# Kernel tuning notes

Hardware: AMD Instinct MI355X
Metric: run time of the kernel (lower is better)

Reference implementation:

```python
import jax, jax.numpy as jnp
import numpy as np
from jax import lax

VOCAB, EMB, HID, NCLS, BATCH, SEQ = 32000, 512, 512, 8, 64, 512


def setup_inputs() -> dict:
    key = jax.random.key(0)
    ks = jax.random.split(key, 12)
    s = 0.05
    return {
        "x": jax.random.randint(ks[0], (BATCH, SEQ), 0, VOCAB),
        "emb": jax.random.normal(ks[1], (VOCAB, EMB), jnp.float32) * s,
        "W_ih0": jax.random.normal(ks[2], (HID, EMB), jnp.float32) * s,
        "W_hh0": jax.random.normal(ks[3], (HID, HID), jnp.float32) * s,
        "b_ih0": jax.random.normal(ks[4], (HID,), jnp.float32) * s,
        "b_hh0": jax.random.normal(ks[5], (HID,), jnp.float32) * s,
        "W_ih1": jax.random.normal(ks[6], (HID, HID), jnp.float32) * s,
        "W_hh1": jax.random.normal(ks[7], (HID, HID), jnp.float32) * s,
        "b_ih1": jax.random.normal(ks[8], (HID,), jnp.float32) * s,
        "b_hh1": jax.random.normal(ks[9], (HID,), jnp.float32) * s,
        "fc_W": jax.random.normal(ks[10], (NCLS, HID), jnp.float32) * s,
        "fc_b": jax.random.normal(ks[11], (NCLS,), jnp.float32) * s,
    }


def _rnn_layer(inp, W_ih, W_hh, b_ih, b_hh):
    # inp: [B, S, F]; tanh RNN, batch_first. Precompute input projection once.
    pre = jnp.einsum('bsf,hf->bsh', inp, W_ih) + b_ih + b_hh  # [B,S,H]
    B = inp.shape[0]
    H = W_hh.shape[0]
    h0 = jnp.zeros((B, H), inp.dtype)

    def step(h, p_t):  # p_t: [B,H]
        h = jnp.tanh(p_t + h @ W_hh.T)
        return h, h

    hT, ys = lax.scan(step, h0, pre.transpose(1, 0, 2))  # scan over time
    return ys.transpose(1, 0, 2), hT  # outputs [B,S,H], last hidden [B,H]


def reference(x, emb, W_ih0, W_hh0, b_ih0, b_hh0, W_ih1, W_hh1, b_ih1, b_hh1, fc_W, fc_b):
    xe = emb[x]  # [B,S,E] embedding lookup
    out0, _ = _rnn_layer(xe, W_ih0, W_hh0, b_ih0, b_hh0)
    _, h1 = _rnn_layer(out0, W_ih1, W_hh1, b_ih1, b_hh1)  # hidden[-1]
    return h1 @ fc_W.T + fc_b  # [B, n_class]
```

## Files before the change

kernel.cpp:

```cpp
#include <hip/hip_runtime.h>
#include <stdint.h>


#define BB 64
#define SS 512
#define HH 512

typedef short bf16x8 __attribute__((ext_vector_type(8)));
typedef float f32x4 __attribute__((ext_vector_type(4)));
typedef int i32x4 __attribute__((ext_vector_type(4)));
typedef unsigned int u32;
typedef u32 u32x2 __attribute__((ext_vector_type(2)));

__device__ __forceinline__ unsigned short f2bf(float f) {
  uint32_t u = __builtin_bit_cast(uint32_t, f);
  u += 0x7FFFu + ((u >> 16) & 1u);
  return (unsigned short)(u >> 16);
}
__device__ __forceinline__ float bf2f(unsigned short h) {
  uint32_t u = ((uint32_t)h) << 16;
  return __builtin_bit_cast(float, u);
}
__device__ __forceinline__ int pack2(unsigned short a, unsigned short b) {
  return (int)(unsigned int)a | ((int)(unsigned int)b << 16);
}
__device__ __forceinline__ u32 hipack(u32 a, u32 b) {
  return (a >> 16) | (b & 0xFFFF0000u);
}
__device__ __forceinline__ u32 lopack(u32 a, u32 b) {
  return (a & 0xFFF8u) | ((b & 0xFFF8u) << 16);
}
__device__ __forceinline__ bool tag4(i32x4 v, u32 t) {
  u32 m = (((u32)v[0] ^ t) | ((u32)v[1] ^ t) | ((u32)v[2] ^ t) | ((u32)v[3] ^ t)) & 7u;
  return m == 0u;
}
__device__ __forceinline__ float fast_tanh(float v) {
  float a = __builtin_fabsf(v);
  float e = __expf(-2.0f * a);
  float t = (1.0f - e) / (1.0f + e);
  return __builtin_copysignf(t, v);
}

#define UC_LOAD4(dst, ptr) \
  asm volatile("global_load_dwordx4 %0, %1, off sc0 sc1" : "=v"(dst) : "v"(ptr))
#define UC_LOAD1(dst, ptr) \
  asm volatile("global_load_dword %0, %1, off sc0 sc1" : "=v"(dst) : "v"(ptr))
#define UC_STORE2(ptr, v) \
  asm volatile("global_store_dwordx2 %0, %1, off sc0 sc1" ::"v"(ptr), "v"(v) : "memory")

#define ISSUE8(a0, a1, a2, a3, a4, a5, a6, a7, base)  \
  do {                                                \
    UC_LOAD4(a0, (base) + 8 * gch + 0);               \
    UC_LOAD4(a1, (base) + 8 * gch + 4);               \
    UC_LOAD4(a2, (base) + 8 * gch + 128);             \
    UC_LOAD4(a3, (base) + 8 * gch + 132);             \
    UC_LOAD4(a4, (base) + 8 * gch + 256);             \
    UC_LOAD4(a5, (base) + 8 * gch + 260);             \
    UC_LOAD4(a6, (base) + 8 * gch + 384);             \
    UC_LOAD4(a7, (base) + 8 * gch + 388);             \
  } while (0)

#define TAGOK8(a0, a1, a2, a3, a4, a5, a6, a7, t)                         \
  (tag4(a0, t) && tag4(a1, t) && tag4(a2, t) && tag4(a3, t) &&            \
   tag4(a4, t) && tag4(a5, t) && tag4(a6, t) && tag4(a7, t))

#define STAGE_IN0(w0, w1, w2, w3, w4, w5, w6, w7)                          \
  do {                                                                     \
    i32x4 A;                                                               \
    A[0] = (int)hipack(w0[0], w0[1]); A[1] = (int)hipack(w0[2], w0[3]);    \
    A[2] = (int)hipack(w1[0], w1[1]); A[3] = (int)hipack(w1[2], w1[3]);    \
    *(i32x4*)(s_in0 + gr * 512 + (((gch + 0) ^ (gr & 7)) << 3)) = A;       \
    A[0] = (int)hipack(w2[0], w2[1]); A[1] = (int)hipack(w2[2], w2[3]);    \
    A[2] = (int)hipack(w3[0], w3[1]); A[3] = (int)hipack(w3[2], w3[3]);    \
    *(i32x4*)(s_in0 + gr * 512 + (((gch + 16) ^ (gr & 7)) << 3)) = A;      \
    A[0] = (int)hipack(w4[0], w4[1]); A[1] = (int)hipack(w4[2], w4[3]);    \
    A[2] = (int)hipack(w5[0], w5[1]); A[3] = (int)hipack(w5[2], w5[3]);    \
    *(i32x4*)(s_in0 + gr * 512 + (((gch + 32) ^ (gr & 7)) << 3)) = A;      \
    A[0] = (int)hipack(w6[0], w6[1]); A[1] = (int)hipack(w6[2], w6[3]);    \
    A[2] = (int)hipack(w7[0], w7[1]); A[3] = (int)hipack(w7[2], w7[3]);    \
    *(i32x4*)(s_in0 + gr * 512 + (((gch + 48) ^ (gr & 7)) << 3)) = A;      \
  } while (0)

#define STAGE_H(w0, w1, w2, w3, w4, w5, w6, w7)                            \
  do {                                                                     \
    i32x4 A, B;                                                            \
    A[0] = (int)hipack(w0[0], w0[1]); A[1] = (int)hipack(w0[2], w0[3]);    \
    A[2] = (int)hipack(w1[0], w1[1]); A[3] = (int)hipack(w1[2], w1[3]);    \
    B[0] = (int)lopack(w0[0], w0[1]); B[1] = (int)lopack(w0[2], w0[3]);    \
    B[2] = (int)lopack(w1[0], w1[1]); B[3] = (int)lopack(w1[2], w1[3]);    \
    *(i32x4*)(s_Hhi + gr * 512 + (((gch + 0) ^ (gr & 7)) << 3)) = A;       \
    *(i32x4*)(s_Hlo + gr * 512 + (((gch + 0) ^ (gr & 7)) << 3)) = B;       \
    A[0] = (int)hipack(w2[0], w2[1]); A[1] = (int)hipack(w2[2], w2[3]);    \
    A[2] = (int)hipack(w3[0], w3[1]); A[3] = (int)hipack(w3[2], w3[3]);    \
    B[0] = (int)lopack(w2[0], w2[1]); B[1] = (int)lopack(w2[2], w2[3]);    \
    B[2] = (int)lopack(w3[0], w3[1]); B[3] = (int)lopack(w3[2], w3[3]);    \
    *(i32x4*)(s_Hhi + gr * 512 + (((gch + 16) ^ (gr & 7)) << 3)) = A;      \
    *(i32x4*)(s_Hlo + gr * 512 + (((gch + 16) ^ (gr & 7)) << 3)) = B;      \
    A[0] = (int)hipack(w4[0], w4[1]); A[1] = (int)hipack(w4[2], w4[3]);    \
    A[2] = (int)hipack(w5[0], w5[1]); A[3] = (int)hipack(w5[2], w5[3]);    \
    B[0] = (int)lopack(w4[0], w4[1]); B[1] = (int)lopack(w4[2], w4[3]);    \
    B[2] = (int)lopack(w5[0], w5[1]); B[3] = (int)lopack(w5[2], w5[3]);    \
    *(i32x4*)(s_Hhi + gr * 512 + (((gch + 32) ^ (gr & 7)) << 3)) = A;      \
    *(i32x4*)(s_Hlo + gr * 512 + (((gch + 32) ^ (gr & 7)) << 3)) = B;      \
    A[0] = (int)hipack(w6[0], w6[1]); A[1] = (int)hipack(w6[2], w6[3]);    \
    A[2] = (int)hipack(w7[0], w7[1]); A[3] = (int)hipack(w7[2], w7[3]);    \
    B[0] = (int)lopack(w6[0], w6[1]); B[1] = (int)lopack(w6[2], w6[3]);    \
    B[2] = (int)lopack(w7[0], w7[1]); B[3] = (int)lopack(w7[2], w7[3]);    \
    *(i32x4*)(s_Hhi + gr * 512 + (((gch + 48) ^ (gr & 7)) << 3)) = A;      \
    *(i32x4*)(s_Hlo + gr * 512 + (((gch + 48) ^ (gr & 7)) << 3)) = B;      \
  } while (0)

__global__ __launch_bounds__(512, 1) void k_rnn(
    const int* __restrict__ x, const float* __restrict__ emb,
    const float* __restrict__ Wih0, const float* __restrict__ Whh0,
    const float* __restrict__ bih0, const float* __restrict__ bhh0,
    const float* __restrict__ Wih1, const float* __restrict__ Whh1,
    const float* __restrict__ bih1, const float* __restrict__ bhh1,
    u32* __restrict__ hsl) {
  const int tid = threadIdx.x;
  const int bid = blockIdx.x;
  const int layer = bid >> 5;
  const int lb = bid & 31;
  const int bg = lb >> 3;
  const int c = lb & 7;
  const int wid = tid >> 6;
  const int lane = tid & 63;
  const int kq = wid >> 1;
  const int nh = wid & 1;
  const int gt = tid & 255;
  const int gr = gt >> 4;
  const int gch = gt & 15;

  __shared__ __align__(16) unsigned short s_in0[16 * 512];
  __shared__ __align__(16) unsigned short s_Hhi[16 * 512];
  __shared__ __align__(16) unsigned short s_Hlo[16 * 512];
  __shared__ __align__(16) float s_part[4 * 16 * 64];

  const float* Wih = layer ? Wih1 : Wih0;
  const float* Whh = layer ? Whh1 : Whh0;
  const float* bi = layer ? bih1 : bih0;
  const float* bh = layer ? bhh1 : bhh0;

  bf16x8 wih[2][4], whhh[2][4], whhl[2][4];
  {
    const int r16 = lane & 15, kg = lane >> 4;
#pragma unroll
    for (int nt = 0; nt < 2; ++nt) {
#pragma unroll
      for (int kt = 0; kt < 4; ++kt) {
        int row = c * 64 + nh * 32 + nt * 16 + r16;
        int k0 = kq * 128 + kt * 32 + kg * 8;
        const float* p = Wih + row * 512 + k0;
        bf16x8 v;
#pragma unroll
        for (int j = 0; j < 8; ++j) v[j] = (short)f2bf(p[j]);
        wih[nt][kt] = v;
        const float* q = Whh + row * 512 + k0;
        bf16x8 vh, vl;
#pragma unroll
        for (int j = 0; j < 8; ++j) {
          float f = q[j];
          unsigned short h = f2bf(f);
          vh[j] = (short)h;
          vl[j] = (short)f2bf(f - bf2f(h));
        }
        whhh[nt][kt] = vh;
        whhl[nt][kt] = vl;
      }
    }
  }
  float biasv0, biasv1;
  {
    int na = (tid & 31) * 2;
    biasv0 = bi[c * 64 + na] + bh[c * 64 + na];
    biasv1 = bi[c * 64 + na + 1] + bh[c * 64 + na + 1];
  }

  float4 pf0, pf1, pf2, pf3, pf4, pf5, pf6, pf7;
  if (layer == 0 && wid < 4) {
    int rid = x[(bg * 16 + gr) * SS + 0];
    const float4* ep = (const float4*)(emb + (size_t)rid * 512);
    pf0 = ep[2 * gch + 0];  pf1 = ep[2 * gch + 1];
    pf2 = ep[2 * gch + 32]; pf3 = ep[2 * gch + 33];
    pf4 = ep[2 * gch + 64]; pf5 = ep[2 * gch + 65];
    pf6 = ep[2 * gch + 96]; pf7 = ep[2 * gch + 97];
  }

  for (int s = 1; s <= SS; ++s) {
    const u32 exp_h = (u32)((s - 1) & 7);

    if (wid < 4) {
      if (layer == 0) {
        {
          i32x4 v;
          v[0] = pack2(f2bf(pf0.x), f2bf(pf0.y));
          v[1] = pack2(f2bf(pf0.z), f2bf(pf0.w));
          v[2] = pack2(f2bf(pf1.x), f2bf(pf1.y));
          v[3] = pack2(f2bf(pf1.z), f2bf(pf1.w));
          *(i32x4*)(s_in0 + gr * 512 + (((gch + 0) ^ (gr & 7)) << 3)) = v;
          v[0] = pack2(f2bf(pf2.x), f2bf(pf2.y));
          v[1] = pack2(f2bf(pf2.z), f2bf(pf2.w));
          v[2] = pack2(f2bf(pf3.x), f2bf(pf3.y));
          v[3] = pack2(f2bf(pf3.z), f2bf(pf3.w));
          *(i32x4*)(s_in0 + gr * 512 + (((gch + 16) ^ (gr & 7)) << 3)) = v;
          v[0] = pack2(f2bf(pf4.x), f2bf(pf4.y));
          v[1] = pack2(f2bf(pf4.z), f2bf(pf4.w));
          v[2] = pack2(f2bf(pf5.x), f2bf(pf5.y));
          v[3] = pack2(f2bf(pf5.z), f2bf(pf5.w));
          *(i32x4*)(s_in0 + gr * 512 + (((gch + 32) ^ (gr & 7)) << 3)) = v;
          v[0] = pack2(f2bf(pf6.x), f2bf(pf6.y));
          v[1] = pack2(f2bf(pf6.z), f2bf(pf6.w));
          v[2] = pack2(f2bf(pf7.x), f2bf(pf7.y));
          v[3] = pack2(f2bf(pf7.z), f2bf(pf7.w));
          *(i32x4*)(s_in0 + gr * 512 + (((gch + 48) ^ (gr & 7)) << 3)) = v;
        }
        if (s < SS) {
          int rid = x[(bg * 16 + gr) * SS + s];
          const float4* ep = (const float4*)(emb + (size_t)rid * 512);
          pf0 = ep[2 * gch + 0];  pf1 = ep[2 * gch + 1];
          pf2 = ep[2 * gch + 32]; pf3 = ep[2 * gch + 33];
          pf4 = ep[2 * gch + 64]; pf5 = ep[2 * gch + 65];
          pf6 = ep[2 * gch + 96]; pf7 = ep[2 * gch + 97];
        }
      } else {
        i32x4 x0 = {0,0,0,0}, x1 = {0,0,0,0}, x2 = {0,0,0,0}, x3 = {0,0,0,0};
        i32x4 x4 = {0,0,0,0}, x5 = {0,0,0,0}, x6 = {0,0,0,0}, x7 = {0,0,0,0};
        i32x4 y0 = {0,0,0,0}, y1 = {0,0,0,0}, y2 = {0,0,0,0}, y3 = {0,0,0,0};
        i32x4 y4 = {0,0,0,0}, y5 = {0,0,0,0}, y6 = {0,0,0,0}, y7 = {0,0,0,0};
        const u32 exp_i = (u32)(s & 7);
        const u32* pib =
            hsl + (((size_t)(s & 3)) * 64 + bg * 16 + gr) * 512;
        ISSUE8(x0, x1, x2, x3, x4, x5, x6, x7, pib);
        ISSUE8(y0, y1, y2, y3, y4, y5, y6, y7, pib);
        bool use_x;
        while (true) {
          asm volatile("s_waitcnt vmcnt(8)"
                       : "+v"(x0), "+v"(x1), "+v"(x2), "+v"(x3), "+v"(x4),
                         "+v"(x5), "+v"(x6), "+v"(x7)::"memory");
          if (__all(TAGOK8(x0, x1, x2, x3, x4, x5, x6, x7, exp_i))) {
            use_x = true;
            break;
          }
          ISSUE8(x0, x1, x2, x3, x4, x5, x6, x7, pib);
          asm volatile("s_waitcnt vmcnt(8)"
                       : "+v"(y0), "+v"(y1), "+v"(y2), "+v"(y3), "+v"(y4),
                         "+v"(y5), "+v"(y6), "+v"(y7)::"memory");
          if (__all(TAGOK8(y0, y1, y2, y3, y4, y5, y6, y7, exp_i))) {
            use_x = false;
            break;
          }
          ISSUE8(y0, y1, y2, y3, y4, y5, y6, y7, pib);
        }
        asm volatile("s_waitcnt vmcnt(0)"
                     : "+v"(x0), "+v"(x1), "+v"(x2), "+v"(x3), "+v"(x4),
                       "+v"(x5), "+v"(x6), "+v"(x7), "+v"(y0), "+v"(y1),
                       "+v"(y2), "+v"(y3), "+v"(y4), "+v"(y5), "+v"(y6),
                       "+v"(y7)::"memory");
        if (use_x) {
          STAGE_IN0(x0, x1, x2, x3, x4, x5, x6, x7);
        } else {
          STAGE_IN0(y0, y1, y2, y3, y4, y5, y6, y7);
        }
      }
    } else {
      if (s > 1) {
        i32x4 x0 = {0,0,0,0}, x1 = {0,0,0,0}, x2 = {0,0,0,0}, x3 = {0,0,0,0};
        i32x4 x4 = {0,0,0,0}, x5 = {0,0,0,0}, x6 = {0,0,0,0}, x7 = {0,0,0,0};
        i32x4 y0 = {0,0,0,0}, y1 = {0,0,0,0}, y2 = {0,0,0,0}, y3 = {0,0,0,0};
        i32x4 y4 = {0,0,0,0}, y5 = {0,0,0,0}, y6 = {0,0,0,0}, y7 = {0,0,0,0};
        const u32* phb = hsl +
            (((size_t)layer * 4 + ((s - 1) & 3)) * 64 + bg * 16 + gr) * 512;
        bool use_x;
        if (layer == 0) {
          const bool need_bp = (s > 4) && (gt < 8);
          const u32 exp_bp = (u32)((s - 4) & 7);
          const u32* pbp = hsl + ((size_t)(4 + ((s - 4) & 3)) * 64 + bg * 16) * 512 +
                           (gt < 8 ? gt * 64 : 0);
          u32 bpx = 0, bpy = 0;
          ISSUE8(x0, x1, x2, x3, x4, x5, x6, x7, phb);
          UC_LOAD1(bpx, pbp);
          ISSUE8(y0, y1, y2, y3, y4, y5, y6, y7, phb);
          UC_LOAD1(bpy, pbp);
          while (true) {
            asm volatile("s_waitcnt vmcnt(9)"
                         : "+v"(x0), "+v"(x1), "+v"(x2), "+v"(x3), "+v"(x4),
                           "+v"(x5), "+v"(x6), "+v"(x7), "+v"(bpx)::"memory");
            if (__all(TAGOK8(x0, x1, x2, x3, x4, x5, x6, x7, exp_h) &&
                      (!need_bp || ((bpx & 7u) == exp_bp)))) {
              use_x = true;
              break;
            }
            ISSUE8(x0, x1, x2, x3, x4, x5, x6, x7, phb);
            UC_LOAD1(bpx, pbp);
            asm volatile("s_waitcnt vmcnt(9)"
                         : "+v"(y0), "+v"(y1), "+v"(y2), "+v"(y3), "+v"(y4),
                           "+v"(y5), "+v"(y6), "+v"(y7), "+v"(bpy)::"memory");
            if (__all(TAGOK8(y0, y1, y2, y3, y4, y5, y6, y7, exp_h) &&
                      (!need_bp || ((bpy & 7u) == exp_bp)))) {
              use_x = false;
              break;
            }
            ISSUE8(y0, y1, y2, y3, y4, y5, y6, y7, phb);
            UC_LOAD1(bpy, pbp);
          }
          asm volatile("s_waitcnt vmcnt(0)"
                       : "+v"(x0), "+v"(x1), "+v"(x2), "+v"(x3), "+v"(x4),
                         "+v"(x5), "+v"(x6), "+v"(x7), "+v"(y0), "+v"(y1),
                         "+v"(y2), "+v"(y3), "+v"(y4), "+v"(y5), "+v"(y6),
                         "+v"(y7), "+v"(bpx), "+v"(bpy)::"memory");
        } else {
          ISSUE8(x0, x1, x2, x3, x4, x5, x6, x7, phb);
          ISSUE8(y0, y1, y2, y3, y4, y5, y6, y7, phb);
          while (true) {
            asm volatile("s_waitcnt vmcnt(8)"
                         : "+v"(x0), "+v"(x1), "+v"(x2), "+v"(x3), "+v"(x4),
                           "+v"(x5), "+v"(x6), "+v"(x7)::"memory");
            if (__all(TAGOK8(x0, x1, x2, x3, x4, x5, x6, x7, exp_h))) {
              use_x = true;
              break;
            }
            ISSUE8(x0, x1, x2, x3, x4, x5, x6, x7, phb);
            asm volatile("s_waitcnt vmcnt(8)"
                         : "+v"(y0), "+v"(y1), "+v"(y2), "+v"(y3), "+v"(y4),
                           "+v"(y5), "+v"(y6), "+v"(y7)::"memory");
            if (__all(TAGOK8(y0, y1, y2, y3, y4, y5, y6, y7, exp_h))) {
              use_x = false;
              break;
            }
            ISSUE8(y0, y1, y2, y3, y4, y5, y6, y7, phb);
          }
          asm volatile("s_waitcnt vmcnt(0)"
                       : "+v"(x0), "+v"(x1), "+v"(x2), "+v"(x3), "+v"(x4),
                         "+v"(x5), "+v"(x6), "+v"(x7), "+v"(y0), "+v"(y1),
                         "+v"(y2), "+v"(y3), "+v"(y4), "+v"(y5), "+v"(y6),
                         "+v"(y7)::"memory");
        }
        if (use_x) {
          STAGE_H(x0, x1, x2, x3, x4, x5, x6, x7);
        } else {
          STAGE_H(y0, y1, y2, y3, y4, y5, y6, y7);
        }
      }
    }
    __syncthreads();

    f32x4 acc0 = {0.f, 0.f, 0.f, 0.f};
    f32x4 acc1 = {0.f, 0.f, 0.f, 0.f};
    {
      const int r16 = lane & 15, kg = lane >> 4;
#pragma unroll
      for (int kt = 0; kt < 4; ++kt) {
        int k8 = kq * 16 + kt * 4 + kg;
        bf16x8 ain = __builtin_bit_cast(
            bf16x8, *(const i32x4*)(s_in0 + r16 * 512 + ((k8 ^ (r16 & 7)) << 3)));
        acc0 = __builtin_amdgcn_mfma_f32_16x16x32_bf16(ain, wih[0][kt], acc0, 0, 0, 0);
        acc1 = __builtin_amdgcn_mfma_f32_16x16x32_bf16(ain, wih[1][kt], acc1, 0, 0, 0);
      }
      if (s > 1) {
#pragma unroll
        for (int kt = 0; kt < 4; ++kt) {
          int k8 = kq * 16 + kt * 4 + kg;
          bf16x8 ahi = __builtin_bit_cast(
              bf16x8, *(const i32x4*)(s_Hhi + r16 * 512 + ((k8 ^ (r16 & 7)) << 3)));
          bf16x8 alo = __builtin_bit_cast(
              bf16x8, *(const i32x4*)(s_Hlo + r16 * 512 + ((k8 ^ (r16 & 7)) << 3)));
          acc0 = __builtin_amdgcn_mfma_f32_16x16x32_bf16(ahi, whhh[0][kt], acc0, 0, 0, 0);
          acc0 = __builtin_amdgcn_mfma_f32_16x16x32_bf16(ahi, whhl[0][kt], acc0, 0, 0, 0);
          acc0 = __builtin_amdgcn_mfma_f32_16x16x32_bf16(alo, whhh[0][kt], acc0, 0, 0, 0);
          acc1 = __builtin_amdgcn_mfma_f32_16x16x32_bf16(ahi, whhh[1][kt], acc1, 0, 0, 0);
          acc1 = __builtin_amdgcn_mfma_f32_16x16x32_bf16(ahi, whhl[1][kt], acc1, 0, 0, 0);
          acc1 = __builtin_amdgcn_mfma_f32_16x16x32_bf16(alo, whhh[1][kt], acc1, 0, 0, 0);
        }
      }
#pragma unroll
      for (int j = 0; j < 4; ++j) {
        int m = kg * 4 + j;
        int xr = (m >> 2) & 3;
        int n0i = nh * 32 + 0 * 16 + r16;
        int n1i = nh * 32 + 1 * 16 + r16;
        s_part[kq * 1024 + m * 64 + (n0i ^ (xr << 4))] = acc0[j];
        s_part[kq * 1024 + m * 64 + (n1i ^ (xr << 4))] = acc1[j];
      }
    }
    __syncthreads();

    {
      int m = tid >> 5, na = (tid & 31) * 2;
      int xr = (m >> 2) & 3;
      float v0 = biasv0, v1 = biasv1;
#pragma unroll
      for (int q2 = 0; q2 < 4; ++q2) {
        const float2* sp =
            (const float2*)(s_part + q2 * 1024 + m * 64 + (na ^ (xr << 4)));
        float2 t = *sp;
        v0 += t.x;
        v1 += t.y;
      }
      v0 = fast_tanh(v0);
      v1 = fast_tanh(v1);
      unsigned short a0 = f2bf(v0), a1 = f2bf(v1);
      unsigned short b0 = f2bf(v0 - bf2f(a0)), b1 = f2bf(v1 - bf2f(a1));
      u32 tag = (u32)(s & 7);
      u32x2 wv;
      wv[0] = ((u32)a0 << 16) | ((u32)b0 & 0xFFF8u) | tag;
      wv[1] = ((u32)a1 << 16) | ((u32)b1 & 0xFFF8u) | tag;
      u32* dst = hsl + (((size_t)layer * 4 + (s & 3)) * 64 + bg * 16 + m) * 512 +
                 c * 64 + na;
      UC_STORE2(dst, wv);
    }
  }
}

__global__ void k_fc(const u32* __restrict__ h1w, const float* __restrict__ fcW,
                     const float* __restrict__ fcb, float* __restrict__ out) {
  int i = threadIdx.x;
  int b = i >> 3, cc = i & 7;
  float acc = fcb[cc];
  const u32* ph = h1w + b * 512;
  const float* pw = fcW + cc * 512;
  for (int k = 0; k < 512; k += 4) {
    int4 w4 = *(const int4*)(ph + k);
    float4 wv = *(const float4*)(pw + k);
    acc += (bf2f((unsigned short)((u32)w4.x >> 16)) +
            bf2f((unsigned short)((u32)w4.x & 0xFFF8u))) * wv.x;
    acc += (bf2f((unsigned short)((u32)w4.y >> 16)) +
            bf2f((unsigned short)((u32)w4.y & 0xFFF8u))) * wv.y;
    acc += (bf2f((unsigned short)((u32)w4.z >> 16)) +
            bf2f((unsigned short)((u32)w4.z & 0xFFF8u))) * wv.z;
    acc += (bf2f((unsigned short)((u32)w4.w >> 16)) +
            bf2f((unsigned short)((u32)w4.w & 0xFFF8u))) * wv.w;
  }
  out[b * 8 + cc] = acc;
}

extern "C" void kernel_launch(void* const* d_in, const int* in_sizes, int n_in,
                              void* d_out, int out_size, void* d_ws, size_t ws_size,
                              hipStream_t stream) {
  const int* x = (const int*)d_in[0];
  const float* emb = (const float*)d_in[1];
  const float* Wih0 = (const float*)d_in[2];
  const float* Whh0 = (const float*)d_in[3];
  const float* bih0 = (const float*)d_in[4];
  const float* bhh0 = (const float*)d_in[5];
  const float* Wih1 = (const float*)d_in[6];
  const float* Whh1 = (const float*)d_in[7];
  const float* bih1 = (const float*)d_in[8];
  const float* bhh1 = (const float*)d_in[9];
  const float* fcW = (const float*)d_in[10];
  const float* fcb = (const float*)d_in[11];

  u32* hsl = (u32*)d_ws;

  hipMemsetAsync(hsl, 0, (size_t)2 * 4 * 64 * 512 * 4, stream);
  hipLaunchKernelGGL(k_rnn, dim3(64), dim3(512), 0, stream, x, emb, Wih0, Whh0,
                     bih0, bhh0, Wih1, Whh1, bih1, bhh1, hsl);
  hipLaunchKernelGGL(k_fc, dim3(1), dim3(512), 0, stream,
                     hsl + (size_t)4 * 64 * 512, fcW, fcb, (float*)d_out);
}
```

Before: 1.910 ms.

## Poll small per-row sentinel words before bulk-loading tagged hidden state

Replaces the double-buffered speculative polling of full 8x16-byte tagged payloads with a two-phase wait. Threads first spin on one sentinel word per publisher slice, then issue the bulk load once and re-check its tags. This is meant to cut the memory traffic and vector-register pressure of repeatedly reloading whole hidden rows while waiting on other blocks. The cost is an extra serialized round trip after the sentinels become ready, which adds latency to every timestep on the critical recurrence path.

```diff
diff --git a/kernel.cpp b/kernel.cpp
--- a/kernel.cpp
+++ b/kernel.cpp
@@ -130,6 +130,8 @@
   const int gt = tid & 255;
   const int gr = gt >> 4;
   const int gch = gt & 15;
+  const int s_row = (wid & 3) * 4 + ((lane & 31) >> 3);
+  const int s_pub = lane & 7;
 
   __shared__ __align__(16) unsigned short s_in0[16 * 512];
   __shared__ __align__(16) unsigned short s_Hhi[16 * 512];
@@ -223,123 +225,61 @@
           pf6 = ep[2 * gch + 96]; pf7 = ep[2 * gch + 97];
         }
       } else {
-        i32x4 x0 = {0,0,0,0}, x1 = {0,0,0,0}, x2 = {0,0,0,0}, x3 = {0,0,0,0};
-        i32x4 x4 = {0,0,0,0}, x5 = {0,0,0,0}, x6 = {0,0,0,0}, x7 = {0,0,0,0};
-        i32x4 y0 = {0,0,0,0}, y1 = {0,0,0,0}, y2 = {0,0,0,0}, y3 = {0,0,0,0};
-        i32x4 y4 = {0,0,0,0}, y5 = {0,0,0,0}, y6 = {0,0,0,0}, y7 = {0,0,0,0};
         const u32 exp_i = (u32)(s & 7);
         const u32* pib =
             hsl + (((size_t)(s & 3)) * 64 + bg * 16 + gr) * 512;
-        ISSUE8(x0, x1, x2, x3, x4, x5, x6, x7, pib);
-        ISSUE8(y0, y1, y2, y3, y4, y5, y6, y7, pib);
-        bool use_x;
+        {
+          const u32* psent =
+              hsl + (((size_t)(s & 3)) * 64 + bg * 16 + s_row) * 512 + s_pub * 64;
+          u32 sw = 0;
+          while (true) {
+            UC_LOAD1(sw, psent);
+            asm volatile("s_waitcnt vmcnt(0)" : "+v"(sw)::"memory");
+            if (__all((sw & 7u) == exp_i)) break;
+          }
+        }
+        i32x4 w0 = {0,0,0,0}, w1 = {0,0,0,0}, w2 = {0,0,0,0}, w3 = {0,0,0,0};
+        i32x4 w4 = {0,0,0,0}, w5 = {0,0,0,0}, w6 = {0,0,0,0}, w7 = {0,0,0,0};
         while (true) {
-          asm volatile("s_waitcnt vmcnt(8)"
-                       : "+v"(x0), "+v"(x1), "+v"(x2), "+v"(x3), "+v"(x4),
-                         "+v"(x5), "+v"(x6), "+v"(x7)::"memory");
-          if (__all(TAGOK8(x0, x1, x2, x3, x4, x5, x6, x7, exp_i))) {
-            use_x = true;
-            break;
-          }
-          ISSUE8(x0, x1, x2, x3, x4, x5, x6, x7, pib);
-          asm volatile("s_waitcnt vmcnt(8)"
-                       : "+v"(y0), "+v"(y1), "+v"(y2), "+v"(y3), "+v"(y4),
-                         "+v"(y5), "+v"(y6), "+v"(y7)::"memory");
-          if (__all(TAGOK8(y0, y1, y2, y3, y4, y5, y6, y7, exp_i))) {
-            use_x = false;
-            break;
-          }
-          ISSUE8(y0, y1, y2, y3, y4, y5, y6, y7, pib);
-        }
-        asm volatile("s_waitcnt vmcnt(0)"
-                     : "+v"(x0), "+v"(x1), "+v"(x2), "+v"(x3), "+v"(x4),
-                       "+v"(x5), "+v"(x6), "+v"(x7), "+v"(y0), "+v"(y1),
-                       "+v"(y2), "+v"(y3), "+v"(y4), "+v"(y5), "+v"(y6),
-                       "+v"(y7)::"memory");
-        if (use_x) {
-          STAGE_IN0(x0, x1, x2, x3, x4, x5, x6, x7);
-        } else {
-          STAGE_IN0(y0, y1, y2, y3, y4, y5, y6, y7);
-        }
+          ISSUE8(w0, w1, w2, w3, w4, w5, w6, w7, pib);
+          asm volatile("s_waitcnt vmcnt(0)"
+                       : "+v"(w0), "+v"(w1), "+v"(w2), "+v"(w3), "+v"(w4),
+                         "+v"(w5), "+v"(w6), "+v"(w7)::"memory");
+          if (__all(TAGOK8(w0, w1, w2, w3, w4, w5, w6, w7, exp_i))) break;
+        }
+        STAGE_IN0(w0, w1, w2, w3, w4, w5, w6, w7);
       }
     } else {
       if (s > 1) {
-        i32x4 x0 = {0,0,0,0}, x1 = {0,0,0,0}, x2 = {0,0,0,0}, x3 = {0,0,0,0};
-        i32x4 x4 = {0,0,0,0}, x5 = {0,0,0,0}, x6 = {0,0,0,0}, x7 = {0,0,0,0};
-        i32x4 y0 = {0,0,0,0}, y1 = {0,0,0,0}, y2 = {0,0,0,0}, y3 = {0,0,0,0};
-        i32x4 y4 = {0,0,0,0}, y5 = {0,0,0,0}, y6 = {0,0,0,0}, y7 = {0,0,0,0};
         const u32* phb = hsl +
             (((size_t)layer * 4 + ((s - 1) & 3)) * 64 + bg * 16 + gr) * 512;
-        bool use_x;
-        if (layer == 0) {
-          const bool need_bp = (s > 4) && (gt < 8);
+        {
+          const u32* psent = hsl +
+              (((size_t)layer * 4 + ((s - 1) & 3)) * 64 + bg * 16 + s_row) * 512 +
+              s_pub * 64;
+          const bool need_bp = (layer == 0) && (s > 4);
           const u32 exp_bp = (u32)((s - 4) & 7);
           const u32* pbp = hsl + ((size_t)(4 + ((s - 4) & 3)) * 64 + bg * 16) * 512 +
-                           (gt < 8 ? gt * 64 : 0);
-          u32 bpx = 0, bpy = 0;
-          ISSUE8(x0, x1, x2, x3, x4, x5, x6, x7, phb);
-          UC_LOAD1(bpx, pbp);
-          ISSUE8(y0, y1, y2, y3, y4, y5, y6, y7, phb);
-          UC_LOAD1(bpy, pbp);
+                           s_pub * 64;
+          u32 sw = 0, bw = 0;
           while (true) {
-            asm volatile("s_waitcnt vmcnt(9)"
-                         : "+v"(x0), "+v"(x1), "+v"(x2), "+v"(x3), "+v"(x4),
-                           "+v"(x5), "+v"(x6), "+v"(x7), "+v"(bpx)::"memory");
-            if (__all(TAGOK8(x0, x1, x2, x3, x4, x5, x6, x7, exp_h) &&
-                      (!need_bp || ((bpx & 7u) == exp_bp)))) {
-              use_x = true;
-              break;
-            }
-            ISSUE8(x0, x1, x2, x3, x4, x5, x6, x7, phb);
-            UC_LOAD1(bpx, pbp);
-            asm volatile("s_waitcnt vmcnt(9)"
-                         : "+v"(y0), "+v"(y1), "+v"(y2), "+v"(y3), "+v"(y4),
-                           "+v"(y5), "+v"(y6), "+v"(y7), "+v"(bpy)::"memory");
-            if (__all(TAGOK8(y0, y1, y2, y3, y4, y5, y6, y7, exp_h) &&
-                      (!need_bp || ((bpy & 7u) == exp_bp)))) {
-              use_x = false;
-              break;
-            }
-            ISSUE8(y0, y1, y2, y3, y4, y5, y6, y7, phb);
-            UC_LOAD1(bpy, pbp);
+            UC_LOAD1(sw, psent);
+            if (need_bp) UC_LOAD1(bw, pbp);
+            asm volatile("s_waitcnt vmcnt(0)" : "+v"(sw), "+v"(bw)::"memory");
+            bool ok = ((sw & 7u) == exp_h) && (!need_bp || ((bw & 7u) == exp_bp));
+            if (__all(ok)) break;
           }
+        }
+        i32x4 w0 = {0,0,0,0}, w1 = {0,0,0,0}, w2 = {0,0,0,0}, w3 = {0,0,0,0};
+        i32x4 w4 = {0,0,0,0}, w5 = {0,0,0,0}, w6 = {0,0,0,0}, w7 = {0,0,0,0};
+        while (true) {
+          ISSUE8(w0, w1, w2, w3, w4, w5, w6, w7, phb);
           asm volatile("s_waitcnt vmcnt(0)"
-                       : "+v"(x0), "+v"(x1), "+v"(x2), "+v"(x3), "+v"(x4),
-                         "+v"(x5), "+v"(x6), "+v"(x7), "+v"(y0), "+v"(y1),
-                         "+v"(y2), "+v"(y3), "+v"(y4), "+v"(y5), "+v"(y6),
-                         "+v"(y7), "+v"(bpx), "+v"(bpy)::"memory");
-        } else {
-          ISSUE8(x0, x1, x2, x3, x4, x5, x6, x7, phb);
-          ISSUE8(y0, y1, y2, y3, y4, y5, y6, y7, phb);
-          while (true) {
-            asm volatile("s_waitcnt vmcnt(8)"
-                         : "+v"(x0), "+v"(x1), "+v"(x2), "+v"(x3), "+v"(x4),
-                           "+v"(x5), "+v"(x6), "+v"(x7)::"memory");
-            if (__all(TAGOK8(x0, x1, x2, x3, x4, x5, x6, x7, exp_h))) {
-              use_x = true;
-              break;
-            }
-            ISSUE8(x0, x1, x2, x3, x4, x5, x6, x7, phb);
-            asm volatile("s_waitcnt vmcnt(8)"
-                         : "+v"(y0), "+v"(y1), "+v"(y2), "+v"(y3), "+v"(y4),
-                           "+v"(y5), "+v"(y6), "+v"(y7)::"memory");
-            if (__all(TAGOK8(y0, y1, y2, y3, y4, y5, y6, y7, exp_h))) {
-              use_x = false;
-              break;
-            }
-            ISSUE8(y0, y1, y2, y3, y4, y5, y6, y7, phb);
-          }
-          asm volatile("s_waitcnt vmcnt(0)"
-                       : "+v"(x0), "+v"(x1), "+v"(x2), "+v"(x3), "+v"(x4),
-                         "+v"(x5), "+v"(x6), "+v"(x7), "+v"(y0), "+v"(y1),
-                         "+v"(y2), "+v"(y3), "+v"(y4), "+v"(y5), "+v"(y6),
-                         "+v"(y7)::"memory");
-        }
-        if (use_x) {
-          STAGE_H(x0, x1, x2, x3, x4, x5, x6, x7);
-        } else {
-          STAGE_H(y0, y1, y2, y3, y4, y5, y6, y7);
-        }
+                       : "+v"(w0), "+v"(w1), "+v"(w2), "+v"(w3), "+v"(w4),
+                         "+v"(w5), "+v"(w6), "+v"(w7)::"memory");
+          if (__all(TAGOK8(w0, w1, w2, w3, w4, w5, w6, w7, exp_h))) break;
+        }
+        STAGE_H(w0, w1, w2, w3, w4, w5, w6, w7);
       }
     }
     __syncthreads();
```

Result: no change. 1.881 ms (-1.5%).
